# Kernel tuning notes

Hardware: AMD Instinct MI355X
Metric: run time of the kernel (lower is better)

## Reference

```python
import jax, jax.numpy as jnp
import numpy as np

N = 100000      # nodes
E = 1600000     # edges (before self loops)
M = 40          # n_markers
HID = 128       # hidden
HEADS = 4
DH = HID // HEADS  # 32 per-head dim
LAT = 64
NEG_SLOPE = 0.2
EPS = 1e-5


def setup_inputs() -> dict:
    key = jax.random.key(0)
    ks = jax.random.split(key, 20)
    r = lambda k, shape, s=0.05: (jax.random.normal(k, shape, jnp.float32) * s)
    x = jax.random.normal(ks[0], (N, M), jnp.float32)
    edge_index = jax.random.randint(ks[1], (2, E), 0, N, jnp.int64)
    return {
        "x": x,
        "edge_index": edge_index,
        "Wp": r(ks[2], (M, HID)), "bp": jnp.zeros((HID,), jnp.float32),
        "W1l": r(ks[3], (HID, HID)), "W1r": r(ks[4], (HID, HID)),
        "att1": r(ks[5], (HEADS, DH)), "b1": jnp.zeros((HID,), jnp.float32),
        "W2l": r(ks[6], (HID, HID)), "W2r": r(ks[7], (HID, HID)),
        "att2": r(ks[8], (HEADS, DH)), "b2": jnp.zeros((HID,), jnp.float32),
        "g1": jnp.ones((HID,), jnp.float32), "be1": jnp.zeros((HID,), jnp.float32),
        "g2": jnp.ones((HID,), jnp.float32), "be2": jnp.zeros((HID,), jnp.float32),
        "Wo": r(ks[9], (HID, LAT)), "bo": jnp.zeros((LAT,), jnp.float32),
    }


def _layernorm(z, g, b):
    mu = jnp.mean(z, axis=-1, keepdims=True)
    var = jnp.mean(jnp.square(z - mu), axis=-1, keepdims=True)
    return (z - mu) * jax.lax.rsqrt(var + EPS) * g + b


def _gatv2(h, src, dst, Wl, Wr, att, bias):
    # h: [N, HID]; per-head source/target projections (GATv2, share_weights=False)
    hl = (h @ Wl).reshape(N, HEADS, DH)  # messages (source side)
    hr = (h @ Wr).reshape(N, HEADS, DH)  # target side
    # per-edge attention logits: a^T LeakyReLU(hl[src] + hr[dst])
    e = jax.nn.leaky_relu(hl[src] + hr[dst], NEG_SLOPE)      # [Etot, HEADS, DH]
    logits = jnp.einsum('ehd,hd->eh', e, att)                # [Etot, HEADS]
    # segment softmax over edges sharing the same destination node
    m = jax.ops.segment_max(logits, dst, num_segments=N)     # [N, HEADS]
    ex = jnp.exp(logits - m[dst])
    denom = jax.ops.segment_sum(ex, dst, num_segments=N)     # [N, HEADS]
    alpha = ex / denom[dst]                                  # [Etot, HEADS]
    # scatter-aggregate weighted source messages
    out = jax.ops.segment_sum(hl[src] * alpha[:, :, None], dst, num_segments=N)
    return out.reshape(N, HID) + bias


def reference(x, edge_index, Wp, bp, W1l, W1r, att1, b1, W2l, W2r, att2, b2,
              g1, be1, g2, be2, Wo, bo):
    loops = jnp.arange(N, dtype=edge_index.dtype)
    src = jnp.concatenate([edge_index[0], loops])  # PyG adds self loops by default
    dst = jnp.concatenate([edge_index[1], loops])
    h = x @ Wp + bp
    h = _layernorm(jax.nn.gelu(_gatv2(h, src, dst, W1l, W1r, att1, b1), approximate=False) + h, g1, be1)
    h = _layernorm(jax.nn.gelu(_gatv2(h, src, dst, W2l, W2r, att2, b2), approximate=False) + h, g2, be2)
    return h @ Wo + bo
```

## Files before the change

### kernel.cpp

```cpp
#include <hip/hip_runtime.h>
#include <hip/hip_bf16.h>
#include <math.h>

#define NN   100000
#define EE   1600000
#define ETOT 1700000
#define MM   40
#define HID  128
#define LAT  64
#define NB   391
#define CHUNK 4096

typedef unsigned short u16;
typedef unsigned int   u32;
typedef unsigned long long u64;

typedef __attribute__((ext_vector_type(8))) short bf16x8;
typedef __attribute__((ext_vector_type(4))) float f32x4;
typedef __attribute__((ext_vector_type(2))) float f32x2;

__device__ __forceinline__ float bf2f(u16 a) {
    return __uint_as_float(((u32)a) << 16);
}
__device__ __forceinline__ u16 f2bf(float f) {
    u32 u = __float_as_uint(f);
    u32 r = (u + 0x7fffu + ((u >> 16) & 1u)) >> 16;
    return (u16)r;
}
__device__ __forceinline__ f32x2 unpk(u32 u) {
    f32x2 r;
    r.x = __uint_as_float(u << 16);
    r.y = __uint_as_float(u & 0xffff0000u);
    return r;
}
__device__ __forceinline__ float exp2_hw(float x) {
    float d;
    asm("v_exp_f32 %0, %1" : "=v"(d) : "v"(x));
    return d;
}
__device__ __forceinline__ void gload_lds16(const void* g, void* l) {
    __builtin_amdgcn_global_load_lds(
        (const __attribute__((address_space(1))) void*)g,
        (__attribute__((address_space(3))) void*)l, 16, 0, 0);
}
__device__ __forceinline__ float gelu_t(float x) {
    float x2 = x * x;
    float y = x * fmaf(0.0713548162726f, x2, 1.59576912161f);
    return x / (1.f + __expf(-y));
}

#define Vbp   0
#define Vatt1 128
#define Vb1   256
#define Vg1   384
#define Vbe1  512
#define Vatt2 640
#define Vb2   768
#define Vg2   896
#define Vbe2  1024
#define Vbo   1152
#define VTOT  1216

#define BWp   0
#define BW1l  8192
#define BW1r  24576
#define BW2l  40960
#define BW2r  57344
#define BWo   73728
#define BTOT  90112

#define XROWS 100096
#define NXB   25000
#define NVB   5
#define NWB   352

__device__ __forceinline__ int sniff_bf_wave(const u32* __restrict__ x_raw) {
    int lane = threadIdx.x & 63;
    u32 w = x_raw[lane];
    u16 lo = (u16)(w & 0xffffu);
    int e = (lo >> 7) & 0xFF;
    int ok = (e >= 118 && e <= 133) ? 1 : 0;
    u64 b = __ballot(ok);
    return (__popcll(b) >= 48) ? 1 : 0;
}

__device__ __forceinline__ void edge_decode(const int* __restrict__ ei, int is64, int e,
                                            int& src, int& dst) {
    if (e < EE) {
        src = is64 ? ei[2 * e] : ei[e];
        int idx = EE + e;
        dst = is64 ? ei[2 * idx] : ei[idx];
    } else {
        src = e - EE; dst = src;
    }
}

__global__ __launch_bounds__(256) void prep_kernel(
    const void* __restrict__ x, const u32* __restrict__ ei_raw,
    const void* p0, const void* p1, const void* p2, const void* p3, const void* p4,
    const void* p5, const void* p6, const void* p7, const void* p8, const void* p9,
    const void* w0, const void* w1, const void* w2, const void* w3, const void* w4,
    const void* w5,
    u16* __restrict__ xb, float* __restrict__ wv, u16* __restrict__ wbf,
    int* __restrict__ flags, u32* __restrict__ gbucket, u32* __restrict__ dcnt,
    u32* __restrict__ gcur, u32* __restrict__ dcur)
{
    const u32* x_raw = (const u32*)x;
    int isbf = sniff_bf_wave(x_raw);
    int t = threadIdx.x;
    int b = blockIdx.x;

    if (b == 0) {
        if (t < 64) {
            u32 a = ei_raw[2 * t + 1] | ei_raw[129 + 2 * t];
            u64 nz = __ballot(a != 0u);
            if (t == 0) { flags[0] = (nz == 0uLL) ? 1 : 0; flags[1] = isbf; }
        }
        gbucket[t] = 0; gbucket[t + 256] = 0;
        gcur[t] = 0;    gcur[t + 256] = 0;
        if (t < 64) { dcnt[t] = 0; dcur[t] = 0; }
        return;
    }
    if (b <= NXB) {
        int i = (b - 1) * 256 + t;
        int row = i >> 6, k = i & 63;
        u16 v = 0;
        if (k < MM) {
            int src = row * MM + k;
            v = isbf ? ((const u16*)x)[src] : f2bf(((const float*)x)[src]);
        }
        xb[i] = v;
        return;
    }
    if (b <= NXB + NVB) {
        int i = (b - 1 - NXB) * 256 + t;
        if (i >= VTOT) return;
        const int offs[11] = {Vbp, Vatt1, Vb1, Vg1, Vbe1, Vatt2, Vb2, Vg2, Vbe2, Vbo, VTOT};
        const void* ps[10] = {p0,p1,p2,p3,p4,p5,p6,p7,p8,p9};
        int s = 0;
#pragma unroll
        for (int k = 1; k < 10; k++) s += (i >= offs[k]) ? 1 : 0;
        int j = i - offs[s];
        const void* p = ps[s];
        wv[i] = isbf ? bf2f(((const u16*)p)[j]) : ((const float*)p)[j];
        return;
    }
    {
        int i = (b - 1 - NXB - NVB) * 256 + t;
        const int offs[7] = {BWp, BW1l, BW1r, BW2l, BW2r, BWo, BTOT};
        const int Ks[6]   = {40, 128, 128, 128, 128, 128};
        const int Ncs[6]  = {128, 128, 128, 128, 128, 64};
        const int Kps[6]  = {64, 128, 128, 128, 128, 128};
        const void* ps[6] = {w0,w1,w2,w3,w4,w5};
        int s = 0;
#pragma unroll
        for (int k = 1; k < 6; k++) s += (i >= offs[k]) ? 1 : 0;
        int j = i - offs[s];
        int Kp = Kps[s];
        int n = j / Kp, k = j % Kp;
        u16 v = 0;
        if (k < Ks[s] && n < Ncs[s]) {
            const void* p = ps[s];
            int src = k * Ncs[s] + n;
            v = isbf ? ((const u16*)p)[src] : f2bf(((const float*)p)[src]);
        }
        wbf[i] = v;
    }
}

__global__ __launch_bounds__(256) void bucket_hist_kernel(
    const int* __restrict__ ei, const int* __restrict__ flags, u32* __restrict__ gbucket)
{
    __shared__ u32 h[512];
    int t = threadIdx.x;
    h[t] = 0; h[t + 256] = 0;
    __syncthreads();
    int is64 = flags[0];
    int base = blockIdx.x * CHUNK;
#pragma unroll
    for (int j = 0; j < CHUNK / 256; j++) {
        int e = base + j * 256 + t;
        if (e < ETOT) {
            int src, dst;
            edge_decode(ei, is64, e, src, dst);
            atomicAdd(&h[dst >> 8], 1u);
        }
    }
    __syncthreads();
    if (h[t])       atomicAdd(&gbucket[t], h[t]);
    if (h[t + 256]) atomicAdd(&gbucket[t + 256], h[t + 256]);
}

__global__ __launch_bounds__(256) void bin_pass_kernel(
    const int* __restrict__ ei, const int* __restrict__ flags,
    const u32* __restrict__ gbucket, u32* __restrict__ gcur, u64* __restrict__ pairs)
{
    __shared__ u32 bh[512];
    __shared__ u32 boff[512];
    __shared__ u32 bbs[512];
    __shared__ u32 bcur[512];
    __shared__ u32 bsc[512];
    __shared__ u64 stage[CHUNK];
    __shared__ u32 ts[256];

    int t = threadIdx.x;
    bh[t] = 0; bh[t + 256] = 0;
    __syncthreads();
    int is64 = flags[0];
    int base = blockIdx.x * CHUNK;
    int chunk_n = ETOT - base; if (chunk_n > CHUNK) chunk_n = CHUNK;

    u64 epk[CHUNK / 256];
#pragma unroll
    for (int j = 0; j < CHUNK / 256; j++) {
        int e = base + j * 256 + t;
        if (e < ETOT) {
            int src, dst;
            edge_decode(ei, is64, e, src, dst);
            epk[j] = (u64)(u32)src | ((u64)(u32)dst << 32);
            atomicAdd(&bh[dst >> 8], 1u);
        }
    }
    __syncthreads();

    {
        u32 g0v = (2 * t     < NB) ? gbucket[2 * t]     : 0;
        u32 g1v = (2 * t + 1 < NB) ? gbucket[2 * t + 1] : 0;
        u32 ps = g0v + g1v;
        ts[t] = ps; __syncthreads();
        for (int d = 1; d < 256; d <<= 1) {
            u32 v = (t >= d) ? ts[t - d] : 0;
            __syncthreads();
            ts[t] += v;
            __syncthreads();
        }
        u32 ex = ts[t] - ps;
        bsc[2 * t] = ex; bsc[2 * t + 1] = ex + g0v;
    }
    __syncthreads();

    u32 s0 = bh[2 * t], s1 = bh[2 * t + 1];
    u32 tsum = s0 + s1;
    ts[t] = tsum; __syncthreads();
    for (int d = 1; d < 256; d <<= 1) {
        u32 v = (t >= d) ? ts[t - d] : 0;
        __syncthreads();
        ts[t] += v;
        __syncthreads();
    }
    u32 excl = ts[t] - tsum;
    boff[2 * t] = excl; boff[2 * t + 1] = excl + s0;
    bcur[2 * t] = excl; bcur[2 * t + 1] = excl + s0;
    __syncthreads();
    if (t < NB && bh[t]) bbs[t] = bsc[t] + atomicAdd(&gcur[t], bh[t]);
    if (t + 256 < NB && bh[t + 256]) bbs[t + 256] = bsc[t + 256] + atomicAdd(&gcur[t + 256], bh[t + 256]);
    __syncthreads();
#pragma unroll
    for (int j = 0; j < CHUNK / 256; j++) {
        int e = base + j * 256 + t;
        if (e < ETOT) {
            u64 pr = epk[j];
            u32 pos = atomicAdd(&bcur[(u32)(pr >> 32) >> 8], 1u);
            stage[pos] = pr;
        }
    }
    __syncthreads();
    for (int i = t; i < chunk_n; i += 256) {
        u64 pr = stage[i];
        u32 b = (u32)(pr >> 32) >> 8;
        pairs[(size_t)bbs[b] + (i - boff[b])] = pr;
    }
}

__global__ __launch_bounds__(256) void sort_pass_kernel(
    const u64* __restrict__ pairs, const u32* __restrict__ gbucket,
    int* __restrict__ srcs, int* __restrict__ offs, u32* __restrict__ dcnt)
{
    __shared__ u32 nh[256];
    __shared__ u32 ns[256];
    __shared__ u32 ncur[256];
    __shared__ u32 dh[64];
    __shared__ u32 bsc[512];
    int t = threadIdx.x;
    int b = blockIdx.x;

    {
        u32 g0v = (2 * t     < NB) ? gbucket[2 * t]     : 0;
        u32 g1v = (2 * t + 1 < NB) ? gbucket[2 * t + 1] : 0;
        u32 ps = g0v + g1v;
        ns[t] = ps; __syncthreads();
        for (int d = 1; d < 256; d <<= 1) {
            u32 v = (t >= d) ? ns[t - d] : 0;
            __syncthreads();
            ns[t] += v;
            __syncthreads();
        }
        u32 ex = ns[t] - ps;
        bsc[2 * t] = ex; bsc[2 * t + 1] = ex + g0v;
    }
    __syncthreads();
    u32 beg = bsc[b], endp = bsc[b + 1];

    nh[t] = 0;
    if (t < 64) dh[t] = 0;
    __syncthreads();
    for (u32 i = beg + t; i < endp; i += 256) {
        u32 dst = (u32)(pairs[i] >> 32);
        atomicAdd(&nh[dst & 255], 1u);
    }
    __syncthreads();
    u32 cnt = nh[t];
    ns[t] = cnt; __syncthreads();
    for (int d = 1; d < 256; d <<= 1) {
        u32 v = (t >= d) ? ns[t - d] : 0;
        __syncthreads();
        ns[t] += v;
        __syncthreads();
    }
    u32 excl = ns[t] - cnt;
    int id = b * 256 + t;
    if (id <= NN) offs[id] = (int)(beg + excl);
    if (id < NN) atomicAdd(&dh[cnt < 63u ? cnt : 63u], 1u);
    ncur[t] = excl;
    __syncthreads();
    if (t < 64 && dh[t]) atomicAdd(&dcnt[t], dh[t]);
    for (u32 i = beg + t; i < endp; i += 256) {
        u64 pr = pairs[i];
        u32 loc = ((u32)(pr >> 32)) & 255;
        u32 p = atomicAdd(&ncur[loc], 1u);
        srcs[beg + p] = (int)(u32)pr;
    }
}

__global__ __launch_bounds__(256) void deg_perm_kernel(
    const int* __restrict__ offs, const u32* __restrict__ dcnt,
    u32* __restrict__ dcur, int* __restrict__ perm)
{
    __shared__ u32 cnt[64];
    __shared__ u32 base[64];
    __shared__ u32 sb[64];
    int t = threadIdx.x;
    if (t < 64) {
        u32 v = dcnt[t];
        u32 x = v;
#pragma unroll
        for (int off = 1; off < 64; off <<= 1) {
            u32 y = __shfl_down(x, off);
            if (t + off < 64) x += y;
        }
        sb[t] = x - v;
        cnt[t] = 0;
    }
    __syncthreads();
    int i = blockIdx.x * 256 + t;
    int d = 0; u32 r = 0;
    bool ok = (i < NN);
    if (ok) {
        d = offs[i + 1] - offs[i];
        if (d > 63) d = 63;
        r = atomicAdd(&cnt[d], 1u);
    }
    __syncthreads();
    if (t < 64 && cnt[t]) base[t] = sb[t] + atomicAdd(&dcur[t], cnt[t]);
    __syncthreads();
    if (ok) perm[base[d] + r] = i;
}

__global__ __launch_bounds__(256) void gemm_proj(
    const u16* __restrict__ A,
    const u16* __restrict__ Bt,
    const float* __restrict__ bias,
    u16* __restrict__ outB)
{
    __shared__ u16 Atile[128 * 64];
    __shared__ u16 Ctile[128 * 136];
    int t = threadIdx.x;
    int wv = t >> 6, lane = t & 63;
    int wx = wv & 1, wy = wv >> 1;
    int l16 = lane & 15, quad = lane >> 4;
    int r0 = blockIdx.x * 128;

    {
        const char* Ab = (const char*)(A + (size_t)r0 * 64);
        char* Lb = (char*)Atile + wv * 4096;
        u32 baseP = (u32)(wv * 4096) + (u32)lane * 16;
#pragma unroll
        for (int j = 0; j < 4; j++) {
            u32 P = baseP + (u32)(j * 1024);
            u32 row = P >> 7;
            u32 L = P ^ ((row & 7u) << 4);
            gload_lds16(Ab + L, Lb + j * 1024);
        }
    }

    f32x4 acc[4][4];
#pragma unroll
    for (int m = 0; m < 4; m++)
#pragma unroll
        for (int n = 0; n < 4; n++) acc[m][n] = (f32x4){0.f, 0.f, 0.f, 0.f};

    int n0 = wy * 64;
    const u16* Bp = Bt + (size_t)(n0 + l16) * 64 + quad * 8;
    const char* At = (const char*)Atile;

    __syncthreads();

#pragma unroll
    for (int k = 0; k < 2; k++) {
        bf16x8 af[4], bfr[4];
#pragma unroll
        for (int n = 0; n < 4; n++)
            bfr[n] = *(const bf16x8*)(Bp + (size_t)n * 16 * 64 + k * 32);
#pragma unroll
        for (int m = 0; m < 4; m++) {
            u32 arow = (u32)(wx * 64 + m * 16 + l16);
            u32 Lb = arow * 128 + (u32)(quad * 16 + k * 64);
            u32 Pb = Lb ^ ((arow & 7u) << 4);
            af[m] = *(const bf16x8*)(At + Pb);
        }
#pragma unroll
        for (int m = 0; m < 4; m++)
#pragma unroll
            for (int n = 0; n < 4; n++)
                acc[m][n] = __builtin_amdgcn_mfma_f32_16x16x32_bf16(af[m], bfr[n], acc[m][n], 0, 0, 0);
    }

#pragma unroll
    for (int m = 0; m < 4; m++) {
#pragma unroll
        for (int n = 0; n < 4; n++) {
            int col = n0 + n * 16 + l16;
            float bb = bias[col];
#pragma unroll
            for (int reg = 0; reg < 4; reg++) {
                int row = wx * 64 + m * 16 + quad * 4 + reg;
                Ctile[row * 136 + col] = f2bf(acc[m][n][reg] + bb);
            }
        }
    }
    __syncthreads();
#pragma unroll
    for (int c = 0; c < 8; c++) {
        int e = (c * 256 + t) * 8;
        int row = e >> 7, col = e & 127;
        int grow = r0 + row;
        if (grow < NN) {
            uint4 v = *(const uint4*)&Ctile[row * 136 + col];
            *(uint4*)&outB[(size_t)grow * 128 + col] = v;
        }
    }
}

__global__ __launch_bounds__(256) void gemm_layer(
    const u16* __restrict__ A,
    const u16* __restrict__ Bt,
    u16* __restrict__ outL, u16* __restrict__ outR)
{
    __shared__ u16 Atile[64 * 128];
    __shared__ u16 Ctile[64 * 264];
    int t = threadIdx.x;
    int wv = t >> 6, lane = t & 63;
    int l16 = lane & 15, quad = lane >> 4;
    int r0 = blockIdx.x * 64;

    {
        const char* Ab = (const char*)(A + (size_t)r0 * 128);
        char* Lb = (char*)Atile + wv * 4096;
        u32 baseP = (u32)(wv * 4096) + (u32)lane * 16;
#pragma unroll
        for (int j = 0; j < 4; j++) {
            u32 P = baseP + (u32)(j * 1024);
            u32 row = P >> 8;
            u32 L = P ^ ((row & 7u) << 4);
            gload_lds16(Ab + L, Lb + j * 1024);
        }
    }

    f32x4 acc[4][4];
#pragma unroll
    for (int m = 0; m < 4; m++)
#pragma unroll
        for (int n = 0; n < 4; n++) acc[m][n] = (f32x4){0.f, 0.f, 0.f, 0.f};

    int n0 = wv * 64;
    const u16* Bp = Bt + (size_t)(n0 + l16) * 128 + quad * 8;
    const char* At = (const char*)Atile;

    __syncthreads();

#pragma unroll
    for (int k = 0; k < 4; k++) {
        bf16x8 af[4], bfr[4];
#pragma unroll
        for (int n = 0; n < 4; n++)
            bfr[n] = *(const bf16x8*)(Bp + (size_t)n * 16 * 128 + k * 32);
#pragma unroll
        for (int m = 0; m < 4; m++) {
            u32 arow = (u32)(m * 16 + l16);
            u32 Lb = arow * 256 + (u32)(quad * 16 + k * 64);
            u32 Pb = Lb ^ ((arow & 7u) << 4);
            af[m] = *(const bf16x8*)(At + Pb);
        }
#pragma unroll
        for (int m = 0; m < 4; m++)
#pragma unroll
            for (int n = 0; n < 4; n++)
                acc[m][n] = __builtin_amdgcn_mfma_f32_16x16x32_bf16(af[m], bfr[n], acc[m][n], 0, 0, 0);
    }

#pragma unroll
    for (int m = 0; m < 4; m++) {
#pragma unroll
        for (int n = 0; n < 4; n++) {
            int col = n0 + n * 16 + l16;
#pragma unroll
            for (int reg = 0; reg < 4; reg++) {
                int row = m * 16 + quad * 4 + reg;
                Ctile[row * 264 + col] = f2bf(acc[m][n][reg]);
            }
        }
    }
    __syncthreads();
#pragma unroll
    for (int c = 0; c < 8; c++) {
        int e = (c * 256 + t) * 8;
        int row = e >> 8, col = e & 255;
        int grow = r0 + row;
        if (grow < NN) {
            uint4 v = *(const uint4*)&Ctile[row * 264 + col];
            if (col < 128) *(uint4*)&outL[(size_t)grow * 128 + col] = v;
            else           *(uint4*)&outR[(size_t)grow * 128 + (col - 128)] = v;
        }
    }
}

__global__ __launch_bounds__(256) void gemm_final(
    const u16* __restrict__ A,
    const u16* __restrict__ Bt,
    const float* __restrict__ bias,
    float* __restrict__ outF, u16* __restrict__ outB,
    const int* __restrict__ flags)
{
    __shared__ u16 Atile[128 * 128];
    __shared__ float Cf[128 * 68];
    int t = threadIdx.x;
    int wv = t >> 6, lane = t & 63;
    int wx = wv & 1, wy = wv >> 1;
    int l16 = lane & 15, quad = lane >> 4;
    int r0 = blockIdx.x * 128;

    {
        const char* Ab = (const char*)(A + (size_t)r0 * 128);
        char* Lb = (char*)Atile + wv * 8192;
        u32 baseP = (u32)(wv * 8192) + (u32)lane * 16;
#pragma unroll
        for (int j = 0; j < 8; j++) {
            u32 P = baseP + (u32)(j * 1024);
            u32 row = P >> 8;
            u32 L = P ^ ((row & 7u) << 4);
            gload_lds16(Ab + L, Lb + j * 1024);
        }
    }

    f32x4 acc[4][2];
#pragma unroll
    for (int m = 0; m < 4; m++)
#pragma unroll
        for (int n = 0; n < 2; n++) acc[m][n] = (f32x4){0.f, 0.f, 0.f, 0.f};

    int n0 = wy * 32;
    const u16* Bp = Bt + (size_t)(n0 + l16) * 128 + quad * 8;
    const char* At = (const char*)Atile;

    __syncthreads();

#pragma unroll
    for (int k = 0; k < 4; k++) {
        bf16x8 af[4], bfr[2];
#pragma unroll
        for (int n = 0; n < 2; n++)
            bfr[n] = *(const bf16x8*)(Bp + (size_t)n * 16 * 128 + k * 32);
#pragma unroll
        for (int m = 0; m < 4; m++) {
            u32 arow = (u32)(wx * 64 + m * 16 + l16);
            u32 Lb = arow * 256 + (u32)(quad * 16 + k * 64);
            u32 Pb = Lb ^ ((arow & 7u) << 4);
            af[m] = *(const bf16x8*)(At + Pb);
        }
#pragma unroll
        for (int m = 0; m < 4; m++)
#pragma unroll
            for (int n = 0; n < 2; n++)
                acc[m][n] = __builtin_amdgcn_mfma_f32_16x16x32_bf16(af[m], bfr[n], acc[m][n], 0, 0, 0);
    }

#pragma unroll
    for (int m = 0; m < 4; m++) {
#pragma unroll
        for (int n = 0; n < 2; n++) {
            int col = n0 + n * 16 + l16;
            float bb = bias[col];
#pragma unroll
            for (int reg = 0; reg < 4; reg++) {
                int row = wx * 64 + m * 16 + quad * 4 + reg;
                Cf[row * 68 + col] = acc[m][n][reg] + bb;
            }
        }
    }
    __syncthreads();
    int mk = flags[1] ? 2 : 1;
#pragma unroll
    for (int c = 0; c < 8; c++) {
        int e = (c * 256 + t) * 4;
        int row = e >> 6, col = e & 63;
        int grow = r0 + row;
        if (grow < NN) {
            f32x4 v = *(const f32x4*)&Cf[row * 68 + col];
            if (mk & 1) {
                *(f32x4*)&outF[(size_t)grow * 64 + col] = v;
            } else {
                uint2 pk;
                pk.x = (u32)f2bf(v.x) | ((u32)f2bf(v.y) << 16);
                pk.y = (u32)f2bf(v.z) | ((u32)f2bf(v.w) << 16);
                *(uint2*)&outB[(size_t)grow * 64 + col] = pk;
            }
        }
    }
}

__global__ __launch_bounds__(256) void gat_agg_kernel(
    const u16* __restrict__ hl, const u16* __restrict__ hr, const u16* __restrict__ hresb,
    const float* __restrict__ att, const float* __restrict__ bias,
    const float* __restrict__ gamma, const float* __restrict__ beta,
    const int* __restrict__ offs, const int* __restrict__ srcs,
    const int* __restrict__ perm,
    u16* __restrict__ outb)
{
    int lane = threadIdx.x & 63;
    int sub = lane >> 4;
    int r = lane & 15;
    int c0 = r * 8;
    u32 cb = (u32)(r << 4);
    int id = (blockIdx.x * 4 + (threadIdx.x >> 6)) * 4 + sub;
    int dst = perm[id];

    int start = offs[dst];
    int deg = offs[dst + 1] - start;
    int dm = deg - 1;
    const char* hlc = (const char*)hl;

    f32x2 hr2[4], av2[4];
    {
        uint4 q = *(const uint4*)((const char*)hr + ((u32)dst << 8) + cb);
        hr2[0] = unpk(q.x); hr2[1] = unpk(q.y); hr2[2] = unpk(q.z); hr2[3] = unpk(q.w);
        const float L2E = 1.4426950408889634f;
        float4 a0 = *(const float4*)&att[c0];
        float4 a1 = *(const float4*)&att[c0 + 4];
        av2[0] = (f32x2){L2E * a0.x, L2E * a0.y}; av2[1] = (f32x2){L2E * a0.z, L2E * a0.w};
        av2[2] = (f32x2){L2E * a1.x, L2E * a1.y}; av2[3] = (f32x2){L2E * a1.z, L2E * a1.w};
    }

    int md = deg;
    md = max(md, __shfl_xor(md, 16));
    md = max(md, __shfl_xor(md, 32));

    f32x2 acc2[4];
#pragma unroll
    for (int i = 0; i < 4; i++) acc2[i] = (f32x2){0.f, 0.f};
    float s = 0.f;

    int sa = srcs[start];
    int sb = srcs[start + (1 < dm ? 1 : dm)];
    uint4 qa = *(const uint4*)(hlc + ((u32)sa << 8) + cb);
    uint4 qb = *(const uint4*)(hlc + ((u32)sb << 8) + cb);
    int sna = srcs[start + (2 < dm ? 2 : dm)];
    int snb = srcs[start + (3 < dm ? 3 : dm)];

    int mi = (md + 1) >> 1;
    for (int j = 0; j < mi; ++j) {
        int e4 = 2 * j + 4, e5 = 2 * j + 5;
        int sna2 = srcs[start + min(e4, dm)];
        int snb2 = srcs[start + min(e5, dm)];
        uint4 qna = *(const uint4*)(hlc + ((u32)sna << 8) + cb);
        uint4 qnb = *(const uint4*)(hlc + ((u32)snb << 8) + cb);

        f32x2 ha[4], hb[4];
        ha[0] = unpk(qa.x); ha[1] = unpk(qa.y); ha[2] = unpk(qa.z); ha[3] = unpk(qa.w);
        hb[0] = unpk(qb.x); hb[1] = unpk(qb.y); hb[2] = unpk(qb.z); hb[3] = unpk(qb.w);
        f32x2 pa2 = (f32x2){0.f, 0.f};
        f32x2 pb2 = (f32x2){0.f, 0.f};
#pragma unroll
        for (int i = 0; i < 4; i++) {
            f32x2 za = ha[i] + hr2[i];
            f32x2 zb = hb[i] + hr2[i];
            f32x2 la = __builtin_elementwise_max(za, za * 0.2f);
            f32x2 lb = __builtin_elementwise_max(zb, zb * 0.2f);
            pa2 = __builtin_elementwise_fma(av2[i], la, pa2);
            pb2 = __builtin_elementwise_fma(av2[i], lb, pb2);
        }
        float pa = pa2.x + pa2.y;
        float pb = pb2.x + pb2.y;
        pa += __shfl_xor(pa, 1); pb += __shfl_xor(pb, 1);
        pa += __shfl_xor(pa, 2); pb += __shfl_xor(pb, 2);
        int e0 = 2 * j, e1 = 2 * j + 1;
        float wa = (e0 < deg) ? exp2_hw(pa) : 0.f;
        float wb = (e1 < deg) ? exp2_hw(pb) : 0.f;
        s += wa + wb;
        f32x2 wa2 = (f32x2){wa, wa};
        f32x2 wb2 = (f32x2){wb, wb};
#pragma unroll
        for (int i = 0; i < 4; i++)
            acc2[i] = __builtin_elementwise_fma(wa2, ha[i],
                      __builtin_elementwise_fma(wb2, hb[i], acc2[i]));

        qa = qna; qb = qnb; sna = sna2; snb = snb2;
    }

    float inv = 1.f / s;
    float v[8];
    {
        float4 b0 = *(const float4*)&bias[c0];
        float4 b1 = *(const float4*)&bias[c0 + 4];
        float bb[8] = {b0.x,b0.y,b0.z,b0.w,b1.x,b1.y,b1.z,b1.w};
        uint4 qr = *(const uint4*)((const char*)hresb + ((u32)dst << 8) + cb);
        f32x2 rr2[4] = {unpk(qr.x), unpk(qr.y), unpk(qr.z), unpk(qr.w)};
#pragma unroll
        for (int i = 0; i < 4; i++) {
            float t0 = fmaf(acc2[i].x, inv, bb[2*i]);
            float t1 = fmaf(acc2[i].y, inv, bb[2*i+1]);
            v[2*i]   = gelu_t(t0) + rr2[i].x;
            v[2*i+1] = gelu_t(t1) + rr2[i].y;
        }
    }

    float s1 = 0.f, s2 = 0.f;
#pragma unroll
    for (int k = 0; k < 8; k++) { s1 += v[k]; s2 = fmaf(v[k], v[k], s2); }
#pragma unroll
    for (int off = 1; off < 16; off <<= 1) {
        s1 += __shfl_xor(s1, off);
        s2 += __shfl_xor(s2, off);
    }
    float mu  = s1 * (1.f / 128.f);
    float var = s2 * (1.f / 128.f) - mu * mu;
    float rstd = rsqrtf(var + 1e-5f);

    float4 g0 = *(const float4*)&gamma[c0];
    float4 g1 = *(const float4*)&gamma[c0 + 4];
    float4 be0 = *(const float4*)&beta[c0];
    float4 be1 = *(const float4*)&beta[c0 + 4];
    float gg[8] = {g0.x,g0.y,g0.z,g0.w,g1.x,g1.y,g1.z,g1.w};
    float eb[8] = {be0.x,be0.y,be0.z,be0.w,be1.x,be1.y,be1.z,be1.w};
    float o[8];
#pragma unroll
    for (int k = 0; k < 8; k++) o[k] = fmaf((v[k] - mu) * rstd, gg[k], eb[k]);
    uint4 pk;
    pk.x = (u32)f2bf(o[0]) | ((u32)f2bf(o[1]) << 16);
    pk.y = (u32)f2bf(o[2]) | ((u32)f2bf(o[3]) << 16);
    pk.z = (u32)f2bf(o[4]) | ((u32)f2bf(o[5]) << 16);
    pk.w = (u32)f2bf(o[6]) | ((u32)f2bf(o[7]) << 16);
    *(uint4*)((char*)outb + ((u32)dst << 8) + cb) = pk;
}

extern "C" void kernel_launch(void* const* d_in, const int* in_sizes, int n_in,
                              void* d_out, int out_size, void* d_ws, size_t ws_size,
                              hipStream_t stream) {
    const void* x  = d_in[0];
    const int*  ei = (const int*)d_in[1];

    char* ws = (char*)d_ws;
    size_t off = 0;
    auto alloc = [&](size_t bytes) -> void* {
        void* p = ws + off;
        off = (off + bytes + 511) & ~(size_t)511;
        return p;
    };
    u16*   xb      = (u16*)  alloc((size_t)XROWS * 64 * 2);
    float* wv      = (float*)alloc((size_t)VTOT * 4);
    u16*   wbf     = (u16*)  alloc((size_t)BTOT * 2);
    u16*   h0b     = (u16*)  alloc((size_t)(NN + 128) * HID * 2);
    u16*   h1b     = (u16*)  alloc((size_t)(NN + 128) * HID * 2);
    u16*   hlb     = (u16*)  alloc((size_t)(NN + 128) * HID * 2);
    u16*   hrb     = (u16*)  alloc((size_t)(NN + 128) * HID * 2);
    int*   offs    = (int*)  alloc((size_t)(NN + 1) * 4);
    u32*   gbucket = (u32*)  alloc(512 * 4);
    u32*   gcur    = (u32*)  alloc(512 * 4);
    int*   flags   = (int*)  alloc(512);
    int*   srcs    = (int*)  alloc(((size_t)ETOT + 64) * 4);
    u64*   pairs   = (u64*)  alloc((size_t)ETOT * 8);
    u32*   dcnt    = (u32*)  alloc(64 * 4);
    u32*   dcur    = (u32*)  alloc(64 * 4);
    int*   perm    = (int*)  alloc((size_t)NN * 4);

    prep_kernel<<<1 + NXB + NVB + NWB, 256, 0, stream>>>(
        x, (const u32*)ei,
        d_in[3], d_in[6], d_in[7], d_in[12], d_in[13], d_in[10], d_in[11], d_in[14], d_in[15], d_in[17],
        d_in[2], d_in[4], d_in[5], d_in[8], d_in[9], d_in[16],
        xb, wv, wbf, flags, gbucket, dcnt, gcur, dcur);

    const int EB = (ETOT + CHUNK - 1) / CHUNK;
    bucket_hist_kernel<<<EB, 256, 0, stream>>>(ei, flags, gbucket);
    bin_pass_kernel<<<EB, 256, 0, stream>>>(ei, flags, gbucket, gcur, pairs);
    sort_pass_kernel<<<NB, 256, 0, stream>>>(pairs, gbucket, srcs, offs, dcnt);

    deg_perm_kernel<<<NB, 256, 0, stream>>>(offs, dcnt, dcur, perm);

    const int GB = (NN + 127) / 128;
    const int LB = (NN + 63) / 64;
    const int AB = NN / 16;

    gemm_proj<<<GB, 256, 0, stream>>>(xb, wbf + BWp, wv + Vbp, h0b);

    gemm_layer<<<LB, 256, 0, stream>>>(h0b, wbf + BW1l, hlb, hrb);
    gat_agg_kernel<<<AB, 256, 0, stream>>>(hlb, hrb, h0b, wv + Vatt1, wv + Vb1,
                                           wv + Vg1, wv + Vbe1, offs, srcs, perm, h1b);

    gemm_layer<<<LB, 256, 0, stream>>>(h1b, wbf + BW2l, hlb, hrb);
    gat_agg_kernel<<<AB, 256, 0, stream>>>(hlb, hrb, h1b, wv + Vatt2, wv + Vb2,
                                           wv + Vg2, wv + Vbe2, offs, srcs, perm, h0b);

    gemm_final<<<GB, 256, 0, stream>>>(h0b, wbf + BWo, wv + Vbo,
                                       (float*)d_out, (u16*)d_out, flags);
}
```

Before: 384.7 us.

## Fuse edge histogram into prep kernel and stage packed edge pairs

```diff
diff --git a/kernel.cpp b/kernel.cpp
--- a/kernel.cpp
+++ b/kernel.cpp
@@ -10,6 +10,7 @@
 #define LAT  64
 #define NB   391
 #define CHUNK 4096
+#define NEB  416
 
 typedef unsigned short u16;
 typedef unsigned int   u32;
@@ -83,6 +84,12 @@
     u64 b = __ballot(ok);
     return (__popcll(b) >= 48) ? 1 : 0;
 }
+__device__ __forceinline__ int sniff_is64_wave(const u32* __restrict__ ei_raw) {
+    int lane = threadIdx.x & 63;
+    u32 a = ei_raw[2 * lane + 1] | ei_raw[129 + 2 * lane];
+    u64 nz = __ballot(a != 0u);
+    return (nz == 0uLL) ? 1 : 0;
+}
 
 __device__ __forceinline__ void edge_decode(const int* __restrict__ ei, int is64, int e,
                                             int& src, int& dst) {
@@ -102,23 +109,42 @@
     const void* w0, const void* w1, const void* w2, const void* w3, const void* w4,
     const void* w5,
     u16* __restrict__ xb, float* __restrict__ wv, u16* __restrict__ wbf,
-    int* __restrict__ flags, u32* __restrict__ gbucket, u32* __restrict__ dcnt,
-    u32* __restrict__ gcur, u32* __restrict__ dcur)
+    int* __restrict__ flags, u32* __restrict__ gbucket, u64* __restrict__ pairs_lin)
 {
     const u32* x_raw = (const u32*)x;
-    int isbf = sniff_bf_wave(x_raw);
     int t = threadIdx.x;
     int b = blockIdx.x;
 
+    if (b >= 1 + NXB + NVB + NWB) {
+        __shared__ u32 h[512];
+        h[t] = 0; h[t + 256] = 0;
+        __syncthreads();
+        int is64 = sniff_is64_wave(ei_raw);
+        const int* ei = (const int*)ei_raw;
+        int hb = b - (1 + NXB + NVB + NWB);
+        int base = hb * CHUNK;
+#pragma unroll
+        for (int j = 0; j < CHUNK / 256; j++) {
+            int e = base + j * 256 + t;
+            if (e < ETOT) {
+                int src, dst;
+                edge_decode(ei, is64, e, src, dst);
+                pairs_lin[e] = (u64)(u32)src | ((u64)(u32)dst << 32);
+                atomicAdd(&h[dst >> 8], 1u);
+            }
+        }
+        __syncthreads();
+        if (h[t])       atomicAdd(&gbucket[t], h[t]);
+        if (h[t + 256]) atomicAdd(&gbucket[t + 256], h[t + 256]);
+        return;
+    }
+
+    int isbf = sniff_bf_wave(x_raw);
     if (b == 0) {
         if (t < 64) {
-            u32 a = ei_raw[2 * t + 1] | ei_raw[129 + 2 * t];
-            u64 nz = __ballot(a != 0u);
-            if (t == 0) { flags[0] = (nz == 0uLL) ? 1 : 0; flags[1] = isbf; }
-        }
-        gbucket[t] = 0; gbucket[t + 256] = 0;
-        gcur[t] = 0;    gcur[t + 256] = 0;
-        if (t < 64) { dcnt[t] = 0; dcur[t] = 0; }
+            int is64 = sniff_is64_wave(ei_raw);
+            if (t == 0) { flags[0] = is64; flags[1] = isbf; }
+        }
         return;
     }
     if (b <= NXB) {
@@ -168,31 +194,8 @@
     }
 }
 
-__global__ __launch_bounds__(256) void bucket_hist_kernel(
-    const int* __restrict__ ei, const int* __restrict__ flags, u32* __restrict__ gbucket)
-{
-    __shared__ u32 h[512];
-    int t = threadIdx.x;
-    h[t] = 0; h[t + 256] = 0;
-    __syncthreads();
-    int is64 = flags[0];
-    int base = blockIdx.x * CHUNK;
-#pragma unroll
-    for (int j = 0; j < CHUNK / 256; j++) {
-        int e = base + j * 256 + t;
-        if (e < ETOT) {
-            int src, dst;
-            edge_decode(ei, is64, e, src, dst);
-            atomicAdd(&h[dst >> 8], 1u);
-        }
-    }
-    __syncthreads();
-    if (h[t])       atomicAdd(&gbucket[t], h[t]);
-    if (h[t + 256]) atomicAdd(&gbucket[t + 256], h[t + 256]);
-}
-
 __global__ __launch_bounds__(256) void bin_pass_kernel(
-    const int* __restrict__ ei, const int* __restrict__ flags,
+    const u64* __restrict__ pairs_lin,
     const u32* __restrict__ gbucket, u32* __restrict__ gcur, u64* __restrict__ pairs)
 {
     __shared__ u32 bh[512];
@@ -206,7 +209,6 @@
     int t = threadIdx.x;
     bh[t] = 0; bh[t + 256] = 0;
     __syncthreads();
-    int is64 = flags[0];
     int base = blockIdx.x * CHUNK;
     int chunk_n = ETOT - base; if (chunk_n > CHUNK) chunk_n = CHUNK;
 
@@ -215,10 +217,9 @@
     for (int j = 0; j < CHUNK / 256; j++) {
         int e = base + j * 256 + t;
         if (e < ETOT) {
-            int src, dst;
-            edge_decode(ei, is64, e, src, dst);
-            epk[j] = (u64)(u32)src | ((u64)(u32)dst << 32);
-            atomicAdd(&bh[dst >> 8], 1u);
+            u64 pr = pairs_lin[e];
+            epk[j] = pr;
+            atomicAdd(&bh[(u32)(pr >> 32) >> 8], 1u);
         }
     }
     __syncthreads();
@@ -783,24 +784,27 @@
     u16*   hlb     = (u16*)  alloc((size_t)(NN + 128) * HID * 2);
     u16*   hrb     = (u16*)  alloc((size_t)(NN + 128) * HID * 2);
     int*   offs    = (int*)  alloc((size_t)(NN + 1) * 4);
-    u32*   gbucket = (u32*)  alloc(512 * 4);
-    u32*   gcur    = (u32*)  alloc(512 * 4);
+    u32*   zblk    = (u32*)  alloc((512 + 512 + 64 + 64) * 4);
+    u32*   gbucket = zblk;
+    u32*   gcur    = zblk + 512;
+    u32*   dcnt    = zblk + 1024;
+    u32*   dcur    = zblk + 1088;
     int*   flags   = (int*)  alloc(512);
     int*   srcs    = (int*)  alloc(((size_t)ETOT + 64) * 4);
-    u64*   pairs   = (u64*)  alloc((size_t)ETOT * 8);
-    u32*   dcnt    = (u32*)  alloc(64 * 4);
-    u32*   dcur    = (u32*)  alloc(64 * 4);
     int*   perm    = (int*)  alloc((size_t)NN * 4);
 
-    prep_kernel<<<1 + NXB + NVB + NWB, 256, 0, stream>>>(
+    u64*   pairs_lin = (u64*)h1b;
+    u64*   pairs     = (u64*)hlb;
+
+    hipMemsetAsync(zblk, 0, (512 + 512 + 64 + 64) * 4, stream);
+
+    prep_kernel<<<1 + NXB + NVB + NWB + NEB, 256, 0, stream>>>(
         x, (const u32*)ei,
         d_in[3], d_in[6], d_in[7], d_in[12], d_in[13], d_in[10], d_in[11], d_in[14], d_in[15], d_in[17],
         d_in[2], d_in[4], d_in[5], d_in[8], d_in[9], d_in[16],
-        xb, wv, wbf, flags, gbucket, dcnt, gcur, dcur);
-
-    const int EB = (ETOT + CHUNK - 1) / CHUNK;
-    bucket_hist_kernel<<<EB, 256, 0, stream>>>(ei, flags, gbucket);
-    bin_pass_kernel<<<EB, 256, 0, stream>>>(ei, flags, gbucket, gcur, pairs);
+        xb, wv, wbf, flags, gbucket, pairs_lin);
+
+    bin_pass_kernel<<<NEB, 256, 0, stream>>>(pairs_lin, gbucket, gcur, pairs);
     sort_pass_kernel<<<NB, 256, 0, stream>>>(pairs, gbucket, srcs, offs, dcnt);
 
     deg_perm_kernel<<<NB, 256, 0, stream>>>(offs, dcnt, dcur, perm);
```

After: 391.1 us. No clear change (+1.7%).
